# Kernel optimization log

Measured on AMD Instinct MI355X. Metric: run time of the kernel, lower is better.

The kernel has to match this reference:

```python
import jax, jax.numpy as jnp
import numpy as np

N, E, IN_DIM, HID, NUM_CLASSES = 100000, 1600000, 256, 128, 40


def setup_inputs() -> dict:
    key = jax.random.key(0)
    ks = jax.random.split(key, 16)
    f32 = jnp.float32

    def w(k, shape):
        fan_in = shape[0]
        return (jax.random.normal(k, shape, f32) / jnp.sqrt(jnp.asarray(fan_in, f32)))

    x = jax.random.normal(ks[0], (N, IN_DIM), f32)
    edge_index = jax.random.randint(ks[1], (2, E), 0, N, dtype=jnp.int32)
    adj_embed = jax.random.normal(ks[2], (N, HID), f32) * 0.02  # xavier-ish
    return {
        "x": x,
        "edge_index": edge_index,
        "adj_embed": adj_embed,
        "wx1": w(ks[3], (IN_DIM, HID)), "bx1": jnp.zeros((HID,), f32),
        "wx2": w(ks[4], (HID, HID)),    "bx2": jnp.zeros((HID,), f32),
        "wa1": w(ks[5], (HID, HID)),    "ba1": jnp.zeros((HID,), f32),
        "wa2": w(ks[6], (HID, HID)),    "ba2": jnp.zeros((HID,), f32),
        "ww1": w(ks[7], (2 * HID, HID)), "bw1": jnp.zeros((HID,), f32),
        "wc": w(ks[8], (HID, NUM_CLASSES)), "bc": jnp.zeros((NUM_CLASSES,), f32),
    }


def _aggregate_neighbours(edge_index, weights, num_nodes):
    src, dst = edge_index[0], edge_index[1]
    # scatter-sum of gathered rows [E, HID] into [num_nodes, HID]
    agg = jax.ops.segment_sum(weights[src], dst, num_segments=num_nodes)
    deg = jax.ops.segment_sum(jnp.ones_like(dst, dtype=weights.dtype), dst,
                              num_segments=num_nodes)
    deg = jnp.maximum(deg, 1.0)[:, None]
    return agg / deg


def reference(x, edge_index, adj_embed, wx1, bx1, wx2, bx2,
              wa1, ba1, wa2, ba2, ww1, bw1, wc, bc):
    # mlp_x (dropout = identity in eval mode)
    hx = jax.nn.relu(x @ wx1 + bx1) @ wx2 + bx2          # [N, HID]
    # adjacency branch: mean-aggregate learned node embeddings over edges
    ha_raw = _aggregate_neighbours(edge_index, adj_embed, adj_embed.shape[0])
    ha = jax.nn.relu(ha_raw @ wa1 + ba1) @ wa2 + ba2     # [N, HID]
    # mlp_w over concat (num_layers=1 -> single Linear+ReLU)
    combined = jnp.concatenate([hx, ha], axis=1)         # [N, 2*HID]
    h = jax.nn.relu(combined @ ww1 + bw1)                # [N, HID]
    h = jax.nn.relu(h + hx + ha)
    logits = h @ wc + bc                                 # [N, NUM_CLASSES]
    return logits
```

## Files before the change

kernel.cpp:

```cpp
#include <hip/hip_runtime.h>

#define Nn 100000
#define Ee 1600000
#define IND 256
#define HD 128
#define NCLS 40
#define NBLK 391

typedef _Float16 f16;
typedef f16 f16x8 __attribute__((ext_vector_type(8)));
typedef f16 f16x4 __attribute__((ext_vector_type(4)));
typedef float f32x4 __attribute__((ext_vector_type(4)));

extern "C" __global__ void __launch_bounds__(256)
k_hist(const int* __restrict__ ei, int* __restrict__ counts) {
    int e = blockIdx.x * 256 + threadIdx.x;
    if (e < Ee) atomicAdd(&counts[ei[Ee + e]], 1);
}

extern "C" __global__ void __launch_bounds__(256)
k_scan1(const int* __restrict__ counts, int* __restrict__ bsum) {
    __shared__ int s[256];
    int t = threadIdx.x;
    int i = blockIdx.x * 256 + t;
    s[t] = (i < Nn) ? counts[i] : 0;
    __syncthreads();
    for (int d = 128; d > 0; d >>= 1) {
        if (t < d) s[t] += s[t + d];
        __syncthreads();
    }
    if (t == 0) bsum[blockIdx.x] = s[0];
}

extern "C" __global__ void __launch_bounds__(512)
k_scan2(int* __restrict__ bsum) {
    __shared__ int s[512];
    int t = threadIdx.x;
    int v = (t < NBLK) ? bsum[t] : 0;
    s[t] = v;
    __syncthreads();
    for (int d = 1; d < 512; d <<= 1) {
        int x = (t >= d) ? s[t - d] : 0;
        __syncthreads();
        s[t] += x;
        __syncthreads();
    }
    if (t < NBLK) bsum[t] = s[t] - v;
}

extern "C" __global__ void __launch_bounds__(256)
k_scan3(const int* __restrict__ counts, const int* __restrict__ bsum,
        int* __restrict__ offsets) {
    __shared__ int s[256];
    int t = threadIdx.x;
    int i = blockIdx.x * 256 + t;
    int v = (i < Nn) ? counts[i] : 0;
    s[t] = v;
    __syncthreads();
    for (int d = 1; d < 256; d <<= 1) {
        int x = (t >= d) ? s[t - d] : 0;
        __syncthreads();
        s[t] += x;
        __syncthreads();
    }
    if (i < Nn) offsets[i] = bsum[blockIdx.x] + s[t] - v;
    if (i == 0) offsets[Nn] = Ee;
}

extern "C" __global__ void __launch_bounds__(256)
k_scatter(const int* __restrict__ ei, const int* __restrict__ offsets,
          int* __restrict__ counts, int* __restrict__ bucket) {
    int e = blockIdx.x * 256 + threadIdx.x;
    if (e >= Ee) return;
    int dst = ei[Ee + e];
    int r = atomicSub(&counts[dst], 1);
    bucket[offsets[dst] + r - 1] = ei[e];
}

extern "C" __global__ void __launch_bounds__(256)
k_embconv(const float* __restrict__ emb, f16* __restrict__ embh) {
    int i = blockIdx.x * 256 + threadIdx.x;
    const float4* p = (const float4*)emb + (size_t)i * 2;
    float4 a = p[0], b = p[1];
    f16x8 h;
    h[0] = (f16)a.x; h[1] = (f16)a.y; h[2] = (f16)a.z; h[3] = (f16)a.w;
    h[4] = (f16)b.x; h[5] = (f16)b.y; h[6] = (f16)b.z; h[7] = (f16)b.w;
    *(f16x8*)(embh + (size_t)i * 8) = h;
}

extern "C" __global__ void __launch_bounds__(256)
k_wpack(const float* __restrict__ wx1, const float* __restrict__ wx2,
        const float* __restrict__ wa1, const float* __restrict__ wa2,
        const float* __restrict__ ww1, const float* __restrict__ wc,
        f16* __restrict__ wp) {
    int idx = blockIdx.x * 256 + threadIdx.x;
    const float* W;
    int K, base;
    if (idx < 32768)       { W = wx1; K = 256; base = 0; }
    else if (idx < 49152)  { W = wx2; K = 128; base = 32768; }
    else if (idx < 65536)  { W = wa1; K = 128; base = 49152; }
    else if (idx < 81920)  { W = wa2; K = 128; base = 65536; }
    else if (idx < 114688) { W = ww1; K = 256; base = 81920; }
    else {
        int local = idx - 114688;
        int j = local & 7;
        int L = (local >> 3) & 63;
        int kt = (local >> 9) & 3;
        int ft = local / 2048;
        int k = kt * 32 + (L >> 4) * 8 + j;
        int n = ft * 16 + (L & 15);
        wp[idx] = (n < NCLS) ? (f16)wc[k * NCLS + n] : (f16)0.f;
        return;
    }
    int local = idx - base;
    int KT = K >> 5;
    int j = local & 7;
    int L = (local >> 3) & 63;
    int kt = (local >> 9) % KT;
    int ft = local / (512 * KT);
    int k = kt * 32 + (L >> 4) * 8 + j;
    int n = ft * 16 + (L & 15);
    wp[idx] = (f16)W[k * HD + n];
}

extern "C" __global__ void __launch_bounds__(256)
k_gather(const int* __restrict__ offsets, const int* __restrict__ bucket,
         const f16* __restrict__ embh, f16* __restrict__ harawp) {
    int t = threadIdx.x;
    int lane = t & 63;
    int node = blockIdx.x * 4 + (t >> 6);
    int q = lane >> 4;
    int cl = (lane & 15) * 8;

    int beg = offsets[node];
    int end = offsets[node + 1];

    float s[8];
#pragma unroll
    for (int j = 0; j < 8; j++) s[j] = 0.f;

    int i = beg + q;
    for (; i + 4 < end; i += 8) {
        int a0 = bucket[i];
        int a1 = bucket[i + 4];
        f16x8 v0 = *(const f16x8*)(embh + (size_t)a0 * HD + cl);
        f16x8 v1 = *(const f16x8*)(embh + (size_t)a1 * HD + cl);
#pragma unroll
        for (int j = 0; j < 8; j++) s[j] += (float)v0[j] + (float)v1[j];
    }
    if (i < end) {
        int a0 = bucket[i];
        f16x8 v0 = *(const f16x8*)(embh + (size_t)a0 * HD + cl);
#pragma unroll
        for (int j = 0; j < 8; j++) s[j] += (float)v0[j];
    }

#pragma unroll
    for (int j = 0; j < 8; j++) {
        s[j] += __shfl_down(s[j], 32);
        s[j] += __shfl_down(s[j], 16);
    }

    if (lane < 16) {
        float inv = 1.0f / fmaxf((float)(end - beg), 1.0f);
        f16x8 h;
#pragma unroll
        for (int j = 0; j < 8; j++) h[j] = (f16)(s[j] * inv);
        int nt = node >> 4, m = node & 15;
        int kt = lane >> 2, q2 = lane & 3;
        *(f16x8*)(harawp + (((nt * 4 + kt) * 64 + m + 16 * q2) * 8)) = h;
    }
}

extern "C" __global__ void __launch_bounds__(256, 5)
linkx_mlp(const float* __restrict__ x, const f16* __restrict__ harawp,
          const f16* __restrict__ wx1p, const float* __restrict__ bx1,
          const f16* __restrict__ wx2p, const float* __restrict__ bx2,
          const f16* __restrict__ wa1p, const float* __restrict__ ba1,
          const f16* __restrict__ wa2p, const float* __restrict__ ba2,
          const f16* __restrict__ ww1p, const float* __restrict__ bw1,
          const f16* __restrict__ wcp, const float* __restrict__ bc,
          float* __restrict__ out) {
    __shared__ __align__(16) f16 shr[4096];
    __shared__ __align__(16) f16 hxp[4096];
    __shared__ __align__(16) f16 hap[4096];

    const int t = threadIdx.x;
    const int node0 = blockIdx.x * 32;
    const int lane = t & 63;
    const int wid = t >> 6;
    const int mt = wid >> 1;
    const int fh = wid & 1;

    f32x4 acc[4];
    float rreg[4][4];

#define INIT_ACC(BIAS)                                                    \
    _Pragma("unroll")                                                     \
    for (int q = 0; q < 4; q++) {                                         \
        float bv = (BIAS)[(fh * 4 + q) * 16 + (lane & 15)];               \
        acc[q][0] = bv; acc[q][1] = bv; acc[q][2] = bv; acc[q][3] = bv;   \
    }

#define GEMM_K128(APACK, BP)                                                  \
    _Pragma("unroll")                                                         \
    for (int kt = 0; kt < 4; kt++) {                                          \
        f16x8 a = *(const f16x8*)((APACK) + ((mt * 4 + kt) * 64 + lane) * 8); \
        _Pragma("unroll")                                                     \
        for (int q = 0; q < 4; q++) {                                         \
            f16x8 b = *(const f16x8*)((BP) + (((fh*4+q)*4 + kt)*64 + lane)*8);\
            acc[q] = __builtin_amdgcn_mfma_f32_16x16x32_f16(a, b, acc[q], 0, 0, 0); \
        }                                                                     \
    }

#define EPILOGUE(MODE, PDST)                                                  \
    _Pragma("unroll")                                                         \
    for (int q = 0; q < 4; q++) {                                             \
        int f = (fh * 4 + q) * 16 + (lane & 15);                              \
        int kt2 = f >> 5, q2 = (f >> 3) & 3, j2 = f & 7;                      \
        _Pragma("unroll")                                                     \
        for (int r = 0; r < 4; r++) {                                         \
            int n = (lane >> 4) * 4 + r;                                      \
            float v = acc[q][r];                                              \
            if (MODE == 0) v = fmaxf(v, 0.f);                                 \
            if (MODE == 1) rreg[q][r] = v;                                    \
            if (MODE == 2) rreg[q][r] += v;                                   \
            if (MODE == 3) v = fmaxf(fmaxf(v, 0.f) + rreg[q][r], 0.f);        \
            (PDST)[((mt * 4 + kt2) * 64 + n + 16 * q2) * 8 + j2] = (f16)v;    \
        }                                                                     \
    }

    INIT_ACC(bx1)
#pragma unroll
    for (int kt = 0; kt < 8; kt++) {
        const float* xr = x + (size_t)(node0 + mt * 16 + (lane & 15)) * IND
                            + kt * 32 + (lane >> 4) * 8;
        float4 u0 = *(const float4*)(xr);
        float4 u1 = *(const float4*)(xr + 4);
        f16x8 a;
        a[0] = (f16)u0.x; a[1] = (f16)u0.y; a[2] = (f16)u0.z; a[3] = (f16)u0.w;
        a[4] = (f16)u1.x; a[5] = (f16)u1.y; a[6] = (f16)u1.z; a[7] = (f16)u1.w;
#pragma unroll
        for (int q = 0; q < 4; q++) {
            f16x8 b = *(const f16x8*)(wx1p + (((fh*4+q)*8 + kt)*64 + lane)*8);
            acc[q] = __builtin_amdgcn_mfma_f32_16x16x32_f16(a, b, acc[q], 0, 0, 0);
        }
    }
    EPILOGUE(0, shr)
    __syncthreads();

    INIT_ACC(bx2)
    GEMM_K128(shr, wx2p)
    EPILOGUE(1, hxp)
    __syncthreads();

    INIT_ACC(ba1)
    {
        int ntb = (node0 >> 4) + mt;
#pragma unroll
        for (int kt = 0; kt < 4; kt++) {
            f16x8 a = *(const f16x8*)(harawp + ((ntb * 4 + kt) * 64 + lane) * 8);
#pragma unroll
            for (int q = 0; q < 4; q++) {
                f16x8 b = *(const f16x8*)(wa1p + (((fh*4+q)*4 + kt)*64 + lane)*8);
                acc[q] = __builtin_amdgcn_mfma_f32_16x16x32_f16(a, b, acc[q], 0, 0, 0);
            }
        }
    }
    EPILOGUE(0, shr)
    __syncthreads();

    INIT_ACC(ba2)
    GEMM_K128(shr, wa2p)
    EPILOGUE(2, hap)
    __syncthreads();

    INIT_ACC(bw1)
#pragma unroll
    for (int kt = 0; kt < 8; kt++) {
        const f16* ap = (kt < 4) ? (hxp + ((mt * 4 + kt) * 64 + lane) * 8)
                                 : (hap + ((mt * 4 + (kt - 4)) * 64 + lane) * 8);
        f16x8 a = *(const f16x8*)ap;
#pragma unroll
        for (int q = 0; q < 4; q++) {
            f16x8 b = *(const f16x8*)(ww1p + (((fh*4+q)*8 + kt)*64 + lane)*8);
            acc[q] = __builtin_amdgcn_mfma_f32_16x16x32_f16(a, b, acc[q], 0, 0, 0);
        }
    }
    EPILOGUE(3, shr)
    __syncthreads();

    {
        int nft = (fh == 0) ? 2 : 1;
#pragma unroll 2
        for (int ii = 0; ii < nft; ii++) {
            int ft = (ii == 0) ? fh : 2;
            int f = ft * 16 + (lane & 15);
            f32x4 c;
            float bv = (f < NCLS) ? bc[f] : 0.f;
            c[0] = bv; c[1] = bv; c[2] = bv; c[3] = bv;
#pragma unroll
            for (int kt = 0; kt < 4; kt++) {
                f16x8 a = *(const f16x8*)(shr + ((mt * 4 + kt) * 64 + lane) * 8);
                f16x8 b = *(const f16x8*)(wcp + ((ft * 4 + kt) * 64 + lane) * 8);
                c = __builtin_amdgcn_mfma_f32_16x16x32_f16(a, b, c, 0, 0, 0);
            }
            if (f < NCLS) {
#pragma unroll
                for (int r = 0; r < 4; r++) {
                    int n = node0 + mt * 16 + (lane >> 4) * 4 + r;
                    out[(size_t)n * NCLS + f] = c[r];
                }
            }
        }
    }
}

extern "C" void kernel_launch(void* const* d_in, const int* in_sizes, int n_in,
                              void* d_out, int out_size, void* d_ws, size_t ws_size,
                              hipStream_t stream) {
    const float* x   = (const float*)d_in[0];
    const int*   ei  = (const int*)d_in[1];
    const float* emb = (const float*)d_in[2];
    const float* wx1 = (const float*)d_in[3];
    const float* bx1 = (const float*)d_in[4];
    const float* wx2 = (const float*)d_in[5];
    const float* bx2 = (const float*)d_in[6];
    const float* wa1 = (const float*)d_in[7];
    const float* ba1 = (const float*)d_in[8];
    const float* wa2 = (const float*)d_in[9];
    const float* ba2 = (const float*)d_in[10];
    const float* ww1 = (const float*)d_in[11];
    const float* bw1 = (const float*)d_in[12];
    const float* wc  = (const float*)d_in[13];
    const float* bc  = (const float*)d_in[14];
    float* out = (float*)d_out;

    int* ws = (int*)d_ws;
    int* counts  = ws;
    int* offsets = ws + 2 * Nn;
    int* bsum    = ws + 3 * Nn + 16;
    int* bucket  = ws + 3 * Nn + 512;
    f16* wp      = (f16*)(ws + 3 * Nn + 512 + Ee);
    f16* wx1p = wp;
    f16* wx2p = wp + 32768;
    f16* wa1p = wp + 49152;
    f16* wa2p = wp + 65536;
    f16* ww1p = wp + 81920;
    f16* wcp  = wp + 114688;
    f16* harawp = wp + 131072;
    f16* embh   = harawp + (size_t)Nn * HD;

    hipMemsetAsync(ws, 0, (size_t)Nn * sizeof(int), stream);

    k_embconv<<<(Nn * HD / 8) / 256, 256, 0, stream>>>(emb, embh);
    k_hist<<<Ee / 256, 256, 0, stream>>>(ei, counts);
    k_scan1<<<NBLK, 256, 0, stream>>>(counts, bsum);
    k_scan2<<<1, 512, 0, stream>>>(bsum);
    k_scan3<<<NBLK, 256, 0, stream>>>(counts, bsum, offsets);
    k_scatter<<<Ee / 256, 256, 0, stream>>>(ei, offsets, counts, bucket);
    k_wpack<<<472, 256, 0, stream>>>(wx1, wx2, wa1, wa2, ww1, wc, wp);
    k_gather<<<Nn / 4, 256, 0, stream>>>(offsets, bucket, embh, harawp);

    linkx_mlp<<<Nn / 32, 256, 0, stream>>>(x, harawp,
                                           wx1p, bx1, wx2p, bx2,
                                           wa1p, ba1, wa2p, ba2,
                                           ww1p, bw1, wcp, bc, out);
}
```

Measured before the change: 521.5 us.

## Merge prep kernels, wave-cooperative index loads in gather, raise MLP occupancy

Merges the embedding fp16 conversion and weight packing into one prep kernel, saving a launch. In the gather kernel each wave loads up to 64 neighbour indices with one coalesced read and hands them out with shuffles. The inner loop is unrolled to four rows per step to keep more loads in flight, and nodes with degree above 64 fall back to direct index reads. The MLP kernel's launch-bounds occupancy hint goes from 5 to 6 blocks, which may force register spills.

New measurement: 551.4 us. +5.7%, slower.

```diff
diff --git a/kernel.cpp b/kernel.cpp
--- a/kernel.cpp
+++ b/kernel.cpp
@@ -78,22 +78,22 @@
 }
 
 extern "C" __global__ void __launch_bounds__(256)
-k_embconv(const float* __restrict__ emb, f16* __restrict__ embh) {
-    int i = blockIdx.x * 256 + threadIdx.x;
-    const float4* p = (const float4*)emb + (size_t)i * 2;
-    float4 a = p[0], b = p[1];
-    f16x8 h;
-    h[0] = (f16)a.x; h[1] = (f16)a.y; h[2] = (f16)a.z; h[3] = (f16)a.w;
-    h[4] = (f16)b.x; h[5] = (f16)b.y; h[6] = (f16)b.z; h[7] = (f16)b.w;
-    *(f16x8*)(embh + (size_t)i * 8) = h;
-}
-
-extern "C" __global__ void __launch_bounds__(256)
-k_wpack(const float* __restrict__ wx1, const float* __restrict__ wx2,
-        const float* __restrict__ wa1, const float* __restrict__ wa2,
-        const float* __restrict__ ww1, const float* __restrict__ wc,
-        f16* __restrict__ wp) {
+k_prep(const float* __restrict__ wx1, const float* __restrict__ wx2,
+       const float* __restrict__ wa1, const float* __restrict__ wa2,
+       const float* __restrict__ ww1, const float* __restrict__ wc,
+       f16* __restrict__ wp,
+       const float* __restrict__ emb, f16* __restrict__ embh) {
     int idx = blockIdx.x * 256 + threadIdx.x;
+    if (idx >= 120832) {
+        int i = idx - 120832;
+        const float4* p = (const float4*)emb + (size_t)i * 2;
+        float4 a = p[0], b = p[1];
+        f16x8 h;
+        h[0] = (f16)a.x; h[1] = (f16)a.y; h[2] = (f16)a.z; h[3] = (f16)a.w;
+        h[4] = (f16)b.x; h[5] = (f16)b.y; h[6] = (f16)b.z; h[7] = (f16)b.w;
+        *(f16x8*)(embh + (size_t)i * 8) = h;
+        return;
+    }
     const float* W;
     int K, base;
     if (idx < 32768)       { W = wx1; K = 256; base = 0; }
@@ -134,21 +134,44 @@
 
     int beg = offsets[node];
     int end = offsets[node + 1];
+    int deg = end - beg;
+
+    int myidx = (lane < deg) ? bucket[beg + lane] : 0;
 
     float s[8];
 #pragma unroll
     for (int j = 0; j < 8; j++) s[j] = 0.f;
 
-    int i = beg + q;
-    for (; i + 4 < end; i += 8) {
-        int a0 = bucket[i];
-        int a1 = bucket[i + 4];
+    int dlim = (deg < 64) ? deg : 64;
+    int e = q;
+    for (; e + 12 < dlim; e += 16) {
+        int a0 = __shfl(myidx, e);
+        int a1 = __shfl(myidx, e + 4);
+        int a2 = __shfl(myidx, e + 8);
+        int a3 = __shfl(myidx, e + 12);
         f16x8 v0 = *(const f16x8*)(embh + (size_t)a0 * HD + cl);
         f16x8 v1 = *(const f16x8*)(embh + (size_t)a1 * HD + cl);
+        f16x8 v2 = *(const f16x8*)(embh + (size_t)a2 * HD + cl);
+        f16x8 v3 = *(const f16x8*)(embh + (size_t)a3 * HD + cl);
+#pragma unroll
+        for (int j = 0; j < 8; j++)
+            s[j] += ((float)v0[j] + (float)v1[j]) + ((float)v2[j] + (float)v3[j]);
+    }
+    for (; e + 4 < dlim; e += 8) {
+        int a0 = __shfl(myidx, e);
+        int a1 = __shfl(myidx, e + 4);
+        f16x8 v0 = *(const f16x8*)(embh + (size_t)a0 * HD + cl);
+        f16x8 v1 = *(const f16x8*)(embh + (size_t)a1 * HD + cl);
 #pragma unroll
         for (int j = 0; j < 8; j++) s[j] += (float)v0[j] + (float)v1[j];
     }
-    if (i < end) {
+    if (e < dlim) {
+        int a0 = __shfl(myidx, e);
+        f16x8 v0 = *(const f16x8*)(embh + (size_t)a0 * HD + cl);
+#pragma unroll
+        for (int j = 0; j < 8; j++) s[j] += (float)v0[j];
+    }
+    for (int i = beg + 64 + q; i < end; i += 4) {
         int a0 = bucket[i];
         f16x8 v0 = *(const f16x8*)(embh + (size_t)a0 * HD + cl);
 #pragma unroll
@@ -162,7 +185,7 @@
     }
 
     if (lane < 16) {
-        float inv = 1.0f / fmaxf((float)(end - beg), 1.0f);
+        float inv = 1.0f / fmaxf((float)deg, 1.0f);
         f16x8 h;
 #pragma unroll
         for (int j = 0; j < 8; j++) h[j] = (f16)(s[j] * inv);
@@ -172,7 +195,7 @@
     }
 }
 
-extern "C" __global__ void __launch_bounds__(256, 5)
+extern "C" __global__ void __launch_bounds__(256, 6)
 linkx_mlp(const float* __restrict__ x, const f16* __restrict__ harawp,
           const f16* __restrict__ wx1p, const float* __restrict__ bx1,
           const f16* __restrict__ wx2p, const float* __restrict__ bx2,
@@ -353,13 +376,12 @@
 
     hipMemsetAsync(ws, 0, (size_t)Nn * sizeof(int), stream);
 
-    k_embconv<<<(Nn * HD / 8) / 256, 256, 0, stream>>>(emb, embh);
+    k_prep<<<6722, 256, 0, stream>>>(wx1, wx2, wa1, wa2, ww1, wc, wp, emb, embh);
     k_hist<<<Ee / 256, 256, 0, stream>>>(ei, counts);
     k_scan1<<<NBLK, 256, 0, stream>>>(counts, bsum);
     k_scan2<<<1, 512, 0, stream>>>(bsum);
     k_scan3<<<NBLK, 256, 0, stream>>>(counts, bsum, offsets);
     k_scatter<<<Ee / 256, 256, 0, stream>>>(ei, offsets, counts, bucket);
-    k_wpack<<<472, 256, 0, stream>>>(wx1, wx2, wa1, wa2, ww1, wc, wp);
     k_gather<<<Nn / 4, 256, 0, stream>>>(offsets, bucket, embh, harawp);
 
     linkx_mlp<<<Nn / 32, 256, 0, stream>>>(x, harawp,
```
